# Kernel optimization log

Measured on AMD Instinct MI355X. Metric: run time of the kernel, lower is better.

The kernel has to match this reference:

```python
import jax, jax.numpy as jnp
import numpy as np

N_NODES = 100000
N_EDGES = 1600000
IN_FEATS = 256
N_HEADS = 4
OUT_FEATS = 32
NEG_SLOPE = 0.2


def setup_inputs() -> dict:
    key = jax.random.key(0)
    k0, k1, k2, k3, k4, k5 = jax.random.split(key, 6)
    feat = jax.random.normal(k0, (N_NODES, IN_FEATS), dtype=jnp.float32)
    src = jax.random.randint(k1, (N_EDGES,), 0, N_NODES, dtype=jnp.int32)
    dst = jax.random.randint(k2, (N_EDGES,), 0, N_NODES, dtype=jnp.int32)
    # fc.weight: [num_heads*out_feats, in_feats] (torch Linear layout)
    W = jax.random.normal(k3, (N_HEADS * OUT_FEATS, IN_FEATS), dtype=jnp.float32) * 0.05
    attn_l = jax.random.normal(k4, (1, N_HEADS, OUT_FEATS), dtype=jnp.float32) * 0.1
    attn_r = jax.random.normal(k5, (1, N_HEADS, OUT_FEATS), dtype=jnp.float32) * 0.1
    return {"feat": feat, "src": src, "dst": dst, "W": W, "attn_l": attn_l, "attn_r": attn_r}


def reference(feat, src, dst, W, attn_l, attn_r):
    N = feat.shape[0]
    H, D = attn_l.shape[1], attn_l.shape[2]
    # fc projection -> [N, H, D]
    feat_src = (feat @ W.T).reshape(N, H, D)
    el = jnp.sum(feat_src * attn_l, axis=-1)  # [N, H]
    er = jnp.sum(feat_src * attn_r, axis=-1)  # [N, H]
    # per-edge scores: u_add_v then LeakyReLU  -> [E, H]
    e = jax.nn.leaky_relu(el[src] + er[dst], negative_slope=NEG_SLOPE)
    # edge_softmax: segmented softmax over edges grouped by destination node
    emax = jax.ops.segment_max(e, dst, num_segments=N)  # [N, H]
    emax = jnp.where(jnp.isfinite(emax), emax, jnp.zeros_like(emax))
    ee = jnp.exp(e - emax[dst])  # [E, H]
    denom = jax.ops.segment_sum(ee, dst, num_segments=N)  # [N, H]
    a = ee / denom[dst]  # [E, H]
    # u_mul_e + sum aggregation -> [N, H, D]
    m = feat_src[src] * a[:, :, None]  # [E, H, D]
    rst = jax.ops.segment_sum(m, dst, num_segments=N)
    return rst
```

## Files before the change

kernel.cpp:

```cpp
#include <hip/hip_runtime.h>
#include <hip/hip_bf16.h>
#include <math.h>

#define NN 100000
#define NE 1600000
#define INF_ 256
#define NH 4
#define DH 32
#define NHD 128
#define NEG_SLOPE 0.2f

#define NBC 391
#define STRIDEC 4608
#define EPBC 4096
#define NBLK_BIN 391
#define GEMM_BLKS 782
#define SMEM_BYTES 32768

typedef __attribute__((ext_vector_type(8))) short bf16x8;
typedef __attribute__((ext_vector_type(4))) float f32x4;

__device__ __forceinline__ unsigned short f2bf(float f) {
    __hip_bfloat16 b = __float2bfloat16(f);
    return *reinterpret_cast<unsigned short*>(&b);
}

__global__ __launch_bounds__(256) void k_prep0(const float* __restrict__ W,
                                               unsigned short* __restrict__ Wimg,
                                               int* __restrict__ gcur) {
    int t = threadIdx.x;
    int b = blockIdx.x;
    if (b == 16) {
        for (int i = t; i < NBC; i += 256) gcur[i] = 0;
        return;
    }
    int i = b * 256 + t;
    int kt = i >> 9;
    int r = (i >> 2) & 127;
    int g = i & 3;
    int slot = g ^ (r & 7);
    const float* s = &W[(size_t)r * INF_ + kt * 32 + g * 8];
    unsigned short tmp[8];
#pragma unroll
    for (int j = 0; j < 8; j++) tmp[j] = f2bf(s[j]);
    *(bf16x8*)&Wimg[(size_t)kt * 8192 + r * 64 + slot * 8] = *(const bf16x8*)tmp;
}

__global__ __launch_bounds__(256) void k_gemmbin(const float* __restrict__ feat,
                                                 const unsigned short* __restrict__ Wimg,
                                                 const int* __restrict__ src,
                                                 const int* __restrict__ dst,
                                                 const float* __restrict__ al,
                                                 const float* __restrict__ ar,
                                                 unsigned short* __restrict__ fsb,
                                                 float* __restrict__ el,
                                                 float* __restrict__ er,
                                                 int* __restrict__ gcur,
                                                 unsigned* __restrict__ packed) {
    __shared__ __align__(16) char smem[SMEM_BYTES];
    const int t = threadIdx.x;

    if (blockIdx.x < NBLK_BIN) {
        int hb = blockIdx.x;
        unsigned* lrec = (unsigned*)smem;
        unsigned short* lbk = (unsigned short*)(smem + 16384);
        int* lc   = (int*)(smem + 24576);
        int* wb   = lc + NBC;
        int* loff = wb + NBC;
        int* wsum = loff + NBC;
        for (int i = t; i < NBC; i += 256) lc[i] = 0;
        __syncthreads();
        int base = hb * EPBC;
#pragma unroll 4
        for (int j = 0; j < 16; j++) {
            int e = base + j * 256 + t;
            if (e < NE) atomicAdd(&lc[dst[e] >> 8], 1);
        }
        __syncthreads();
        int i0 = t * 2;
        int c0 = (i0 < NBC) ? lc[i0] : 0;
        int c1 = (i0 + 1 < NBC) ? lc[i0 + 1] : 0;
        int s2 = c0 + c1;
        int lane = t & 63, w = t >> 6;
        int x = s2;
#pragma unroll
        for (int o = 1; o < 64; o <<= 1) {
            int y = __shfl_up(x, o);
            if (lane >= o) x += y;
        }
        if (lane == 63) wsum[w] = x;
        __syncthreads();
        int add = 0;
        for (int j = 0; j < w; j++) add += wsum[j];
        int ex = add + x - s2;
        if (i0 < NBC) loff[i0] = ex;
        if (i0 + 1 < NBC) loff[i0 + 1] = ex + c0;
        for (int i = t; i < NBC; i += 256) {
            int c = lc[i];
            wb[i] = c ? i * STRIDEC + atomicAdd(&gcur[i], c) : 0;
        }
        __syncthreads();
        for (int i = t; i < NBC; i += 256) lc[i] = loff[i];
        __syncthreads();
#pragma unroll 4
        for (int j = 0; j < 16; j++) {
            int e = base + j * 256 + t;
            if (e < NE) {
                int d = dst[e];
                int bk = d >> 8;
                int pos = atomicAdd(&lc[bk], 1);
                lrec[pos] = ((unsigned)src[e] << 8) | (unsigned)(d & 255);
                lbk[pos] = (unsigned short)bk;
            }
        }
        __syncthreads();
        int nedge = NE - base;
        if (nedge > EPBC) nedge = EPBC;
        for (int i = t; i < nedge; i += 256) {
            int bk = lbk[i];
            int g = wb[bk] + (i - loff[bk]);
            if (g < (bk + 1) * STRIDEC)
                packed[g] = lrec[i];
        }
        return;
    }

    short* sA = (short*)smem;
    short* sB = (short*)(smem + 16384);
    const int brow = (blockIdx.x - NBLK_BIN) * 128;
    const int wid = t >> 6, lane = t & 63;
    const int wr = wid >> 1, wc = wid & 1;
    const int lg = lane >> 4;
    const int lr = lane & 15;

    f32x4 acc[4][4];
#pragma unroll
    for (int m = 0; m < 4; m++)
#pragma unroll
        for (int n = 0; n < 4; n++) acc[m][n] = (f32x4){0.f, 0.f, 0.f, 0.f};

    const int srow = t >> 1;
    const int cb = (t & 1) * 16;
    const int g0 = cb >> 3;
    const int p0 = (g0 ^ (srow & 7));
    const int p1 = ((g0 + 1) ^ (srow & 7));
    const int grow = brow + srow;
    const bool arow_ok = (grow < NN);
    const char* bimg = (const char*)Wimg;

    float fv[16];
    uint4 wv0, wv1, wv2, wv3;
    if (arow_ok) {
        const float4* pa = (const float4*)&feat[(size_t)grow * INF_ + cb];
        *(float4*)&fv[0] = pa[0];
        *(float4*)&fv[4] = pa[1];
        *(float4*)&fv[8] = pa[2];
        *(float4*)&fv[12] = pa[3];
    } else {
#pragma unroll
        for (int j = 0; j < 16; j++) fv[j] = 0.f;
    }
    wv0 = *(const uint4*)(bimg + t * 16);
    wv1 = *(const uint4*)(bimg + 4096 + t * 16);
    wv2 = *(const uint4*)(bimg + 8192 + t * 16);
    wv3 = *(const uint4*)(bimg + 12288 + t * 16);

    for (int kt = 0; kt < 8; kt++) {
        {
            short sv[16];
#pragma unroll
            for (int j = 0; j < 16; j++) sv[j] = (short)f2bf(fv[j]);
            *(bf16x8*)&sA[srow * 64 + p0 * 8] = *(const bf16x8*)&sv[0];
            *(bf16x8*)&sA[srow * 64 + p1 * 8] = *(const bf16x8*)&sv[8];
            char* bd = (char*)sB;
            *(uint4*)(bd + t * 16) = wv0;
            *(uint4*)(bd + 4096 + t * 16) = wv1;
            *(uint4*)(bd + 8192 + t * 16) = wv2;
            *(uint4*)(bd + 12288 + t * 16) = wv3;
        }
        __syncthreads();
        if (kt < 7) {
            int k0 = (kt + 1) * 32;
            if (arow_ok) {
                const float4* pa = (const float4*)&feat[(size_t)grow * INF_ + k0 + cb];
                *(float4*)&fv[0] = pa[0];
                *(float4*)&fv[4] = pa[1];
                *(float4*)&fv[8] = pa[2];
                *(float4*)&fv[12] = pa[3];
            }
            const char* bsrc = bimg + (size_t)(kt + 1) * 16384;
            wv0 = *(const uint4*)(bsrc + t * 16);
            wv1 = *(const uint4*)(bsrc + 4096 + t * 16);
            wv2 = *(const uint4*)(bsrc + 8192 + t * 16);
            wv3 = *(const uint4*)(bsrc + 12288 + t * 16);
        }
        bf16x8 aF[4], bF[4];
#pragma unroll
        for (int m = 0; m < 4; m++) {
            int r = wr * 64 + m * 16 + lr;
            aF[m] = *(const bf16x8*)&sA[r * 64 + ((lg ^ (r & 7)) * 8)];
        }
#pragma unroll
        for (int n = 0; n < 4; n++) {
            int r = wc * 64 + n * 16 + lr;
            bF[n] = *(const bf16x8*)&sB[r * 64 + ((lg ^ (r & 7)) * 8)];
        }
#pragma unroll
        for (int m = 0; m < 4; m++)
#pragma unroll
            for (int n = 0; n < 4; n++)
                acc[m][n] = __builtin_amdgcn_mfma_f32_16x16x32_bf16(aF[m], bF[n], acc[m][n], 0, 0, 0);
        __syncthreads();
    }
#pragma unroll
    for (int m = 0; m < 4; m++) {
#pragma unroll
        for (int n = 0; n < 4; n++) {
#pragma unroll
            for (int r = 0; r < 4; r++) {
                int gr = brow + wr * 64 + m * 16 + lg * 4 + r;
                if (gr < NN)
                    fsb[(size_t)gr * NHD + wc * 64 + n * 16 + lr] = f2bf(acc[m][n][r]);
            }
        }
    }
    const int hA = wc * 2, hB = wc * 2 + 1;
    const float alA0 = al[hA * 32 + lr], alA1 = al[hA * 32 + 16 + lr];
    const float alB0 = al[hB * 32 + lr], alB1 = al[hB * 32 + 16 + lr];
    const float arA0 = ar[hA * 32 + lr], arA1 = ar[hA * 32 + 16 + lr];
    const float arB0 = ar[hB * 32 + lr], arB1 = ar[hB * 32 + 16 + lr];
#pragma unroll
    for (int m = 0; m < 4; m++) {
#pragma unroll
        for (int r = 0; r < 4; r++) {
            float eA = acc[m][0][r] * alA0 + acc[m][1][r] * alA1;
            float eB = acc[m][2][r] * alB0 + acc[m][3][r] * alB1;
            float fA = acc[m][0][r] * arA0 + acc[m][1][r] * arA1;
            float fB = acc[m][2][r] * arB0 + acc[m][3][r] * arB1;
#pragma unroll
            for (int off = 1; off < 16; off <<= 1) {
                eA += __shfl_xor(eA, off);
                eB += __shfl_xor(eB, off);
                fA += __shfl_xor(fA, off);
                fB += __shfl_xor(fB, off);
            }
            if (lr == 0) {
                int gr = brow + wr * 64 + m * 16 + lg * 4 + r;
                if (gr < NN) {
                    el[gr * 4 + hA] = eA;
                    el[gr * 4 + hB] = eB;
                    er[gr * 4 + hA] = fA;
                    er[gr * 4 + hB] = fB;
                }
            }
        }
    }
}

__global__ __launch_bounds__(256) void k_sort(const int* __restrict__ gcur,
                                              const unsigned* __restrict__ packed,
                                              int* __restrict__ esrc,
                                              int2* __restrict__ rowmeta) {
    __shared__ int lh[256];
    __shared__ int off[256];
    __shared__ int cur[256];
    __shared__ int wsum[4];
    __shared__ int es[STRIDEC];
    int b = blockIdx.x, t = threadIdx.x;
    int beg = b * STRIDEC;
    int cnt = gcur[b];
    if (cnt > STRIDEC) cnt = STRIDEC;

    lh[t] = 0;
    __syncthreads();
    for (int k = t; k < cnt; k += 256)
        atomicAdd(&lh[packed[beg + k] & 255u], 1);
    __syncthreads();
    int v = lh[t];
    int lane = t & 63, w = t >> 6;
    int x = v;
#pragma unroll
    for (int o = 1; o < 64; o <<= 1) {
        int y = __shfl_up(x, o);
        if (lane >= o) x += y;
    }
    if (lane == 63) wsum[w] = x;
    __syncthreads();
    int add = 0;
    for (int j = 0; j < w; j++) add += wsum[j];
    int excl = add + x - v;
    off[t] = excl;
    cur[t] = excl;
    int node = (b << 8) + t;
    if (node < NN) rowmeta[node] = make_int2(beg + excl, v);
    __syncthreads();
    for (int k = t; k < cnt; k += 256) {
        unsigned p = packed[beg + k];
        int pos = atomicAdd(&cur[p & 255u], 1);
        es[pos] = (int)(p >> 8);
    }
    __syncthreads();
    for (int k = t; k < cnt; k += 256) esrc[beg + k] = es[k];
}

__global__ __launch_bounds__(256) void k_agg(const int2* __restrict__ rowmeta,
                                             const int* __restrict__ esrc,
                                             const float* __restrict__ el,
                                             const float* __restrict__ er,
                                             const uint4* __restrict__ fsb128,
                                             float* __restrict__ out) {
    int gid = blockIdx.x * blockDim.x + threadIdx.x;
    int node = gid >> 6;
    int lane = gid & 63;
    if (node >= NN) return;
    int q = lane >> 4;
    int sl = lane & 15;
    int h = sl >> 2;
    int2 md = rowmeta[node];
    int beg = md.x;
    int end = md.x + md.y;
    float rr = er[node * 4 + h];
    float den = 0.f;
    float a0 = 0.f, a1 = 0.f, a2 = 0.f, a3 = 0.f;
    float a4 = 0.f, a5 = 0.f, a6 = 0.f, a7 = 0.f;

#define STEP(eV, vV)                                           \
    {                                                          \
        float sc_ = (eV) + rr;                                 \
        sc_ = sc_ > 0.f ? sc_ : NEG_SLOPE * sc_;               \
        float ee = __expf(sc_);                                \
        den += ee;                                             \
        a0 += ee * __uint_as_float((vV).x << 16);              \
        a1 += ee * __uint_as_float((vV).x & 0xFFFF0000u);      \
        a2 += ee * __uint_as_float((vV).y << 16);              \
        a3 += ee * __uint_as_float((vV).y & 0xFFFF0000u);      \
        a4 += ee * __uint_as_float((vV).z << 16);              \
        a5 += ee * __uint_as_float((vV).z & 0xFFFF0000u);      \
        a6 += ee * __uint_as_float((vV).w << 16);              \
        a7 += ee * __uint_as_float((vV).w & 0xFFFF0000u);      \
    }

    int k = beg + q;
    for (; k + 4 < end; k += 8) {
        int s0 = esrc[k];
        int s1 = esrc[k + 4];
        uint4 v0 = fsb128[(size_t)s0 * 16 + sl];
        uint4 v1 = fsb128[(size_t)s1 * 16 + sl];
        float e0 = el[s0 * 4 + h];
        float e1 = el[s1 * 4 + h];
        STEP(e0, v0)
        STEP(e1, v1)
    }
    for (; k < end; k += 4) {
        int s = esrc[k];
        uint4 v = fsb128[(size_t)s * 16 + sl];
        float eV = el[s * 4 + h];
        STEP(eV, v)
    }
#undef STEP

#pragma unroll
    for (int o = 16; o <= 32; o <<= 1) {
        a0 += __shfl_xor(a0, o);
        a1 += __shfl_xor(a1, o);
        a2 += __shfl_xor(a2, o);
        a3 += __shfl_xor(a3, o);
        a4 += __shfl_xor(a4, o);
        a5 += __shfl_xor(a5, o);
        a6 += __shfl_xor(a6, o);
        a7 += __shfl_xor(a7, o);
        den += __shfl_xor(den, o);
    }

    if (q == 0) {
        float inv = den > 0.f ? 1.0f / den : 0.f;
        float4 o0, o1;
        o0.x = a0 * inv; o0.y = a1 * inv; o0.z = a2 * inv; o0.w = a3 * inv;
        o1.x = a4 * inv; o1.y = a5 * inv; o1.z = a6 * inv; o1.w = a7 * inv;
        float* p = &out[(size_t)node * NHD + sl * 8];
        *(float4*)p = o0;
        *(float4*)(p + 4) = o1;
    }
}

extern "C" void kernel_launch(void* const* d_in, const int* in_sizes, int n_in,
                              void* d_out, int out_size, void* d_ws, size_t ws_size,
                              hipStream_t stream) {
    const float* feat = (const float*)d_in[0];
    const int* src = (const int*)d_in[1];
    const int* dst = (const int*)d_in[2];
    const float* W = (const float*)d_in[3];
    const float* al = (const float*)d_in[4];
    const float* ar = (const float*)d_in[5];
    float* out = (float*)d_out;

    char* ws = (char*)d_ws;
    unsigned short* fsb = (unsigned short*)ws;   ws += (size_t)NN * NHD * 2;
    unsigned* packed = (unsigned*)ws;            ws += (size_t)NBC * STRIDEC * 4;
    int* esrc = (int*)ws;                        ws += (size_t)NBC * STRIDEC * 4;
    float* el = (float*)ws;                      ws += (size_t)NN * NH * 4;
    float* er = (float*)ws;                      ws += (size_t)NN * NH * 4;
    int2* rowmeta = (int2*)ws;                   ws += (size_t)NN * 8;
    int* gcur = (int*)ws;                        ws += (size_t)NBC * 4;
    unsigned short* Wimg = (unsigned short*)ws;  ws += (size_t)8 * 8192 * 2;

    k_prep0<<<17, 256, 0, stream>>>(W, Wimg, gcur);
    k_gemmbin<<<GEMM_BLKS + NBLK_BIN, 256, 0, stream>>>(feat, Wimg, src, dst,
                                                        al, ar, fsb, el, er,
                                                        gcur, packed);
    k_sort<<<NBC, 256, 0, stream>>>(gcur, packed, esrc, rowmeta);
    k_agg<<<(NN * 64 + 255) / 256, 256, 0, stream>>>(rowmeta, esrc, el, er,
                                                     (const uint4*)fsb, out);
}
```

Baseline: 141.1 us.

## Regroup kernels: pair binning with weight prep, and GEMM with per-bucket sort

Edge binning moves out of the GEMM kernel into a new kernel that also converts W to its swizzled bf16 image. The per-bucket counting sort moves into the GEMM launch as extra blocks, so it now overlaps the bandwidth-heavy feature projection instead of running as its own launch. The gcur counter is now zeroed with hipMemsetAsync. The binning phase, which used to overlap the GEMM, now runs alone beforehand, so any gain depends on the sort hiding behind the GEMM better than the binning did.

```diff
diff --git a/kernel.cpp b/kernel.cpp
--- a/kernel.cpp
+++ b/kernel.cpp
@@ -15,7 +15,8 @@
 #define EPBC 4096
 #define NBLK_BIN 391
 #define GEMM_BLKS 782
-#define SMEM_BYTES 32768
+#define PREPBIN_SMEM 29456
+#define GEMMSORT_SMEM 32768
 
 typedef __attribute__((ext_vector_type(8))) short bf16x8;
 typedef __attribute__((ext_vector_type(4))) float f32x4;
@@ -25,64 +26,125 @@
     return *reinterpret_cast<unsigned short*>(&b);
 }
 
-__global__ __launch_bounds__(256) void k_prep0(const float* __restrict__ W,
-                                               unsigned short* __restrict__ Wimg,
-                                               int* __restrict__ gcur) {
-    int t = threadIdx.x;
-    int b = blockIdx.x;
-    if (b == 16) {
-        for (int i = t; i < NBC; i += 256) gcur[i] = 0;
-        return;
-    }
-    int i = b * 256 + t;
-    int kt = i >> 9;
-    int r = (i >> 2) & 127;
-    int g = i & 3;
-    int slot = g ^ (r & 7);
-    const float* s = &W[(size_t)r * INF_ + kt * 32 + g * 8];
-    unsigned short tmp[8];
-#pragma unroll
-    for (int j = 0; j < 8; j++) tmp[j] = f2bf(s[j]);
-    *(bf16x8*)&Wimg[(size_t)kt * 8192 + r * 64 + slot * 8] = *(const bf16x8*)tmp;
-}
-
-__global__ __launch_bounds__(256) void k_gemmbin(const float* __restrict__ feat,
-                                                 const unsigned short* __restrict__ Wimg,
+__global__ __launch_bounds__(256) void k_prepbin(const float* __restrict__ W,
                                                  const int* __restrict__ src,
                                                  const int* __restrict__ dst,
-                                                 const float* __restrict__ al,
-                                                 const float* __restrict__ ar,
-                                                 unsigned short* __restrict__ fsb,
-                                                 float* __restrict__ el,
-                                                 float* __restrict__ er,
+                                                 unsigned short* __restrict__ Wimg,
                                                  int* __restrict__ gcur,
                                                  unsigned* __restrict__ packed) {
-    __shared__ __align__(16) char smem[SMEM_BYTES];
+    __shared__ __align__(16) char smem[PREPBIN_SMEM];
     const int t = threadIdx.x;
 
-    if (blockIdx.x < NBLK_BIN) {
-        int hb = blockIdx.x;
-        unsigned* lrec = (unsigned*)smem;
-        unsigned short* lbk = (unsigned short*)(smem + 16384);
-        int* lc   = (int*)(smem + 24576);
-        int* wb   = lc + NBC;
-        int* loff = wb + NBC;
-        int* wsum = loff + NBC;
-        for (int i = t; i < NBC; i += 256) lc[i] = 0;
-        __syncthreads();
-        int base = hb * EPBC;
+    if (blockIdx.x >= NBLK_BIN) {
+        int i = (blockIdx.x - NBLK_BIN) * 256 + t;
+        int kt = i >> 9;
+        int r = (i >> 2) & 127;
+        int g = i & 3;
+        int slot = g ^ (r & 7);
+        const float* s = &W[(size_t)r * INF_ + kt * 32 + g * 8];
+        unsigned short tmp[8];
+#pragma unroll
+        for (int j = 0; j < 8; j++) tmp[j] = f2bf(s[j]);
+        *(bf16x8*)&Wimg[(size_t)kt * 8192 + r * 64 + slot * 8] = *(const bf16x8*)tmp;
+        return;
+    }
+
+    int hb = blockIdx.x;
+    unsigned* lrec = (unsigned*)smem;
+    unsigned short* lbk = (unsigned short*)(smem + 16384);
+    int* lc   = (int*)(smem + 24576);
+    int* wb   = lc + NBC;
+    int* loff = wb + NBC;
+    int* wsum = loff + NBC;
+    for (int i = t; i < NBC; i += 256) lc[i] = 0;
+    __syncthreads();
+    int base = hb * EPBC;
 #pragma unroll 4
-        for (int j = 0; j < 16; j++) {
-            int e = base + j * 256 + t;
-            if (e < NE) atomicAdd(&lc[dst[e] >> 8], 1);
-        }
-        __syncthreads();
-        int i0 = t * 2;
-        int c0 = (i0 < NBC) ? lc[i0] : 0;
-        int c1 = (i0 + 1 < NBC) ? lc[i0 + 1] : 0;
-        int s2 = c0 + c1;
+    for (int j = 0; j < 16; j++) {
+        int e = base + j * 256 + t;
+        if (e < NE) atomicAdd(&lc[dst[e] >> 8], 1);
+    }
+    __syncthreads();
+    int i0 = t * 2;
+    int c0 = (i0 < NBC) ? lc[i0] : 0;
+    int c1 = (i0 + 1 < NBC) ? lc[i0 + 1] : 0;
+    int s2 = c0 + c1;
+    int lane = t & 63, w = t >> 6;
+    int x = s2;
+#pragma unroll
+    for (int o = 1; o < 64; o <<= 1) {
+        int y = __shfl_up(x, o);
+        if (lane >= o) x += y;
+    }
+    if (lane == 63) wsum[w] = x;
+    __syncthreads();
+    int add = 0;
+    for (int j = 0; j < w; j++) add += wsum[j];
+    int ex = add + x - s2;
+    if (i0 < NBC) loff[i0] = ex;
+    if (i0 + 1 < NBC) loff[i0 + 1] = ex + c0;
+    for (int i = t; i < NBC; i += 256) {
+        int c = lc[i];
+        wb[i] = c ? i * STRIDEC + atomicAdd(&gcur[i], c) : 0;
+    }
+    __syncthreads();
+    for (int i = t; i < NBC; i += 256) lc[i] = loff[i];
+    __syncthreads();
+#pragma unroll 4
+    for (int j = 0; j < 16; j++) {
+        int e = base + j * 256 + t;
+        if (e < NE) {
+            int d = dst[e];
+            int bk = d >> 8;
+            int pos = atomicAdd(&lc[bk], 1);
+            lrec[pos] = ((unsigned)src[e] << 8) | (unsigned)(d & 255);
+            lbk[pos] = (unsigned short)bk;
+        }
+    }
+    __syncthreads();
+    int nedge = NE - base;
+    if (nedge > EPBC) nedge = EPBC;
+    for (int i = t; i < nedge; i += 256) {
+        int bk = lbk[i];
+        int g = wb[bk] + (i - loff[bk]);
+        if (g < (bk + 1) * STRIDEC)
+            packed[g] = lrec[i];
+    }
+}
+
+__global__ __launch_bounds__(256) void k_gemmsort(const float* __restrict__ feat,
+                                                  const unsigned short* __restrict__ Wimg,
+                                                  const float* __restrict__ al,
+                                                  const float* __restrict__ ar,
+                                                  const int* __restrict__ gcur,
+                                                  const unsigned* __restrict__ packed,
+                                                  unsigned short* __restrict__ fsb,
+                                                  float* __restrict__ el,
+                                                  float* __restrict__ er,
+                                                  int* __restrict__ esrc,
+                                                  int2* __restrict__ rowmeta) {
+    __shared__ __align__(16) char smem[GEMMSORT_SMEM];
+    const int t = threadIdx.x;
+
+    if (blockIdx.x >= GEMM_BLKS) {
+        int b = blockIdx.x - GEMM_BLKS;
+        int* lh = (int*)smem;
+        int* off = lh + 256;
+        int* cur = off + 256;
+        int* wsum = cur + 256;
+        int* es = wsum + 4;
+        int beg = b * STRIDEC;
+        int cnt = gcur[b];
+        if (cnt > STRIDEC) cnt = STRIDEC;
+
+        lh[t] = 0;
+        __syncthreads();
+        for (int k = t; k < cnt; k += 256)
+            atomicAdd(&lh[packed[beg + k] & 255u], 1);
+        __syncthreads();
+        int v = lh[t];
         int lane = t & 63, w = t >> 6;
-        int x = s2;
+        int x = v;
 #pragma unroll
         for (int o = 1; o < 64; o <<= 1) {
             int y = __shfl_up(x, o);
@@ -92,42 +154,25 @@
         __syncthreads();
         int add = 0;
         for (int j = 0; j < w; j++) add += wsum[j];
-        int ex = add + x - s2;
-        if (i0 < NBC) loff[i0] = ex;
-        if (i0 + 1 < NBC) loff[i0 + 1] = ex + c0;
-        for (int i = t; i < NBC; i += 256) {
-            int c = lc[i];
-            wb[i] = c ? i * STRIDEC + atomicAdd(&gcur[i], c) : 0;
-        }
-        __syncthreads();
-        for (int i = t; i < NBC; i += 256) lc[i] = loff[i];
-        __syncthreads();
-#pragma unroll 4
-        for (int j = 0; j < 16; j++) {
-            int e = base + j * 256 + t;
-            if (e < NE) {
-                int d = dst[e];
-                int bk = d >> 8;
-                int pos = atomicAdd(&lc[bk], 1);
-                lrec[pos] = ((unsigned)src[e] << 8) | (unsigned)(d & 255);
-                lbk[pos] = (unsigned short)bk;
-            }
-        }
-        __syncthreads();
-        int nedge = NE - base;
-        if (nedge > EPBC) nedge = EPBC;
-        for (int i = t; i < nedge; i += 256) {
-            int bk = lbk[i];
-            int g = wb[bk] + (i - loff[bk]);
-            if (g < (bk + 1) * STRIDEC)
-                packed[g] = lrec[i];
-        }
+        int excl = add + x - v;
+        off[t] = excl;
+        cur[t] = excl;
+        int node = (b << 8) + t;
+        if (node < NN) rowmeta[node] = make_int2(beg + excl, v);
+        __syncthreads();
+        for (int k = t; k < cnt; k += 256) {
+            unsigned p = packed[beg + k];
+            int pos = atomicAdd(&cur[p & 255u], 1);
+            es[pos] = (int)(p >> 8);
+        }
+        __syncthreads();
+        for (int k = t; k < cnt; k += 256) esrc[beg + k] = es[k];
         return;
     }
 
     short* sA = (short*)smem;
     short* sB = (short*)(smem + 16384);
-    const int brow = (blockIdx.x - NBLK_BIN) * 128;
+    const int brow = blockIdx.x * 128;
     const int wid = t >> 6, lane = t & 63;
     const int wr = wid >> 1, wc = wid & 1;
     const int lg = lane >> 4;
@@ -238,11 +283,11 @@
             float fA = acc[m][0][r] * arA0 + acc[m][1][r] * arA1;
             float fB = acc[m][2][r] * arB0 + acc[m][3][r] * arB1;
 #pragma unroll
-            for (int off = 1; off < 16; off <<= 1) {
-                eA += __shfl_xor(eA, off);
-                eB += __shfl_xor(eB, off);
-                fA += __shfl_xor(fA, off);
-                fB += __shfl_xor(fB, off);
+            for (int off2 = 1; off2 < 16; off2 <<= 1) {
+                eA += __shfl_xor(eA, off2);
+                eB += __shfl_xor(eB, off2);
+                fA += __shfl_xor(fA, off2);
+                fB += __shfl_xor(fB, off2);
             }
             if (lr == 0) {
                 int gr = brow + wr * 64 + m * 16 + lg * 4 + r;
@@ -255,52 +300,6 @@
             }
         }
     }
-}
-
-__global__ __launch_bounds__(256) void k_sort(const int* __restrict__ gcur,
-                                              const unsigned* __restrict__ packed,
-                                              int* __restrict__ esrc,
-                                              int2* __restrict__ rowmeta) {
-    __shared__ int lh[256];
-    __shared__ int off[256];
-    __shared__ int cur[256];
-    __shared__ int wsum[4];
-    __shared__ int es[STRIDEC];
-    int b = blockIdx.x, t = threadIdx.x;
-    int beg = b * STRIDEC;
-    int cnt = gcur[b];
-    if (cnt > STRIDEC) cnt = STRIDEC;
-
-    lh[t] = 0;
-    __syncthreads();
-    for (int k = t; k < cnt; k += 256)
-        atomicAdd(&lh[packed[beg + k] & 255u], 1);
-    __syncthreads();
-    int v = lh[t];
-    int lane = t & 63, w = t >> 6;
-    int x = v;
-#pragma unroll
-    for (int o = 1; o < 64; o <<= 1) {
-        int y = __shfl_up(x, o);
-        if (lane >= o) x += y;
-    }
-    if (lane == 63) wsum[w] = x;
-    __syncthreads();
-    int add = 0;
-    for (int j = 0; j < w; j++) add += wsum[j];
-    int excl = add + x - v;
-    off[t] = excl;
-    cur[t] = excl;
-    int node = (b << 8) + t;
-    if (node < NN) rowmeta[node] = make_int2(beg + excl, v);
-    __syncthreads();
-    for (int k = t; k < cnt; k += 256) {
-        unsigned p = packed[beg + k];
-        int pos = atomicAdd(&cur[p & 255u], 1);
-        es[pos] = (int)(p >> 8);
-    }
-    __syncthreads();
-    for (int k = t; k < cnt; k += 256) esrc[beg + k] = es[k];
 }
 
 __global__ __launch_bounds__(256) void k_agg(const int2* __restrict__ rowmeta,
@@ -404,11 +403,11 @@
     int* gcur = (int*)ws;                        ws += (size_t)NBC * 4;
     unsigned short* Wimg = (unsigned short*)ws;  ws += (size_t)8 * 8192 * 2;
 
-    k_prep0<<<17, 256, 0, stream>>>(W, Wimg, gcur);
-    k_gemmbin<<<GEMM_BLKS + NBLK_BIN, 256, 0, stream>>>(feat, Wimg, src, dst,
-                                                        al, ar, fsb, el, er,
-                                                        gcur, packed);
-    k_sort<<<NBC, 256, 0, stream>>>(gcur, packed, esrc, rowmeta);
+    hipMemsetAsync(gcur, 0, (size_t)NBC * sizeof(int), stream);
+    k_prepbin<<<NBLK_BIN + 17, 256, 0, stream>>>(W, src, dst, Wimg, gcur, packed);
+    k_gemmsort<<<GEMM_BLKS + NBC, 256, 0, stream>>>(feat, Wimg, al, ar, gcur,
+                                                    packed, fsb, el, er,
+                                                    esrc, rowmeta);
     k_agg<<<(NN * 64 + 255) / 256, 256, 0, stream>>>(rowmeta, esrc, el, er,
                                                      (const uint4*)fsb, out);
 }
```

Result: slower. 149.4 us (+5.9%).
